# Kernel optimization log

Measured on AMD Instinct MI355X. Metric: run time of the kernel, lower is better.

Reference implementation:

```python
import jax, jax.numpy as jnp
import numpy as np

COMMITMENT_COST = 0.25


def setup_inputs() -> dict:
    key = jax.random.key(0)
    k1, k2 = jax.random.split(key)
    x = jax.random.normal(k1, (32, 256, 32, 32), dtype=jnp.float32)
    codebook = jax.random.normal(k2, (1024, 256), dtype=jnp.float32) * 0.02
    return {"x": x, "codebook": codebook}


def reference(x, codebook):
    # x: [B, C, H, W] -> z: [B, H, W, C] (NHWC), C = embedding_dim
    B, C, H, W = x.shape
    z = jnp.transpose(x, (0, 2, 3, 1))
    zf = z.reshape(-1, C)  # [N, C], N = B*H*W
    # squared euclidean distance: ||z||^2 - 2 z.e + ||e||^2  -> [N, K]
    d = (
        jnp.sum(zf * zf, axis=-1, keepdims=True)
        - 2.0 * (zf @ codebook.T)
        + jnp.sum(codebook * codebook, axis=-1)
    )
    encoding_indices = jnp.argmin(d, axis=1)  # [N]
    quantized = codebook[encoding_indices].reshape(z.shape)  # [B, H, W, C]

    # training losses (entropy_loss_ratio == 0 -> entropy branch skipped)
    sg = jax.lax.stop_gradient
    e_latent_loss = jnp.mean((sg(quantized) - z) ** 2) * COMMITMENT_COST
    q_latent_loss = jnp.mean((quantized - sg(z)) ** 2)
    quantizer_loss = e_latent_loss + q_latent_loss

    # straight-through estimator
    quantized_st = z + sg(quantized - z)
    out = jnp.transpose(quantized_st, (0, 3, 1, 2))  # back to NCHW
    return out, quantizer_loss, e_latent_loss, q_latent_loss, encoding_indices
```

## Files before the change

kernel.cpp:

```cpp
#include <hip/hip_runtime.h>
#include <cfloat>

#define C_DIM   256
#define HW      1024
#define N_ROWS  32768
#define K_CODES 1024
#define ROWS    64
#define NCHUNK  32
#define WCHUNK_BYTES 8192
#define LISTCAP 128
#define DELTA   0.008f
#define CMASK   0xFFFFFFE0u

#define OUT_ELEMS 8388608
#define LOSS_OFF  8388608
#define IDX_OFF   8388611

typedef _Float16 half8 __attribute__((ext_vector_type(8)));
typedef _Float16 f16x4 __attribute__((ext_vector_type(4)));
typedef float    f32x4 __attribute__((ext_vector_type(4)));

#define AS1 __attribute__((address_space(1)))
#define AS3 __attribute__((address_space(3)))

#define OFF_EBUF  0
#define OFF_EN    65536
#define OFF_S32   69632
#define OFF_M1W   69888
#define OFF_THR   70400
#define OFF_RES   70656
#define OFF_FIDX  71168
#define OFF_LCNT  71424
#define OFF_LMETA 71680
#define SMEM_BYTES 73728

#define QT_STRIDE 258

#define DPP_MIN(x, ctrl) fminf((x), __int_as_float(__builtin_amdgcn_update_dpp(0, __float_as_int(x), (ctrl), 0xf, 0xf, true)))

__global__ void prep_kernel(const float* __restrict__ cb, float* __restrict__ enorm,
                            char* __restrict__ cb16) {
    int k = blockIdx.x * 4 + (threadIdx.x >> 6);
    int lane = threadIdx.x & 63;
    int c0 = lane * 4;
    float4 v = *(const float4*)(cb + k * C_DIM + c0);
    double s = (double)v.x * v.x + (double)v.y * v.y + (double)v.z * v.z + (double)v.w * v.w;
    #pragma unroll
    for (int m = 1; m < 64; m <<= 1) s += __shfl_xor(s, m, 64);
    if (lane == 0) enorm[k] = (float)s;
    f16x4 h;
    h[0] = (_Float16)v.x; h[1] = (_Float16)v.y; h[2] = (_Float16)v.z; h[3] = (_Float16)v.w;
    int dst = ((k >> 4) << 13) + ((c0 >> 5) << 10) + (((c0 >> 3) & 3) << 8)
            + ((k & 15) << 4) + ((c0 & 7) << 1);
    *(f16x4*)(cb16 + dst) = h;
}

__global__ __launch_bounds__(256, 2) void vq_main(
    const float* __restrict__ x, const float* __restrict__ cb,
    const float* __restrict__ enorm_g, const char* __restrict__ cb16,
    float* __restrict__ out, float* __restrict__ idx_out, float* __restrict__ t2_out)
{
    extern __shared__ char smem[];
    float* qt      = (float*)(smem + OFF_EBUF);
    float* en_lds  = (float*)(smem + OFF_EN);
    float* S32     = (float*)(smem + OFF_S32);
    float* m1w     = (float*)(smem + OFF_M1W);
    float* thr     = (float*)(smem + OFF_THR);
    unsigned long long* res = (unsigned long long*)(smem + OFF_RES);
    int*   fidx    = (int*)(smem + OFF_FIDX);
    int*   lcnt    = (int*)(smem + OFF_LCNT);
    unsigned int* lmeta = (unsigned int*)(smem + OFF_LMETA);

    const int t    = threadIdx.x;
    const int lane = t & 63;
    const int wv   = t >> 6;
    const int wr   = wv >> 1;
    const int wc   = wv & 1;
    const int l15  = lane & 15;
    const int l4   = lane >> 4;
    const int row0 = blockIdx.x * ROWS;
    const int b    = row0 >> 10;
    const int hw0  = row0 & 1023;
    const float* xb = x + b * (C_DIM * HW) + hw0;

    char* ebw = smem + OFF_EBUF + wv * (2 * WCHUNK_BYTES);
    const char* cbw = cb16 + wc * WCHUNK_BYTES;

    #pragma unroll
    for (int c2 = 0; c2 < 2; c2++) {
        const char* src = cbw + (c2 << 14);
        char* dst = ebw + c2 * WCHUNK_BYTES;
        #pragma unroll
        for (int i = 0; i < 8; i++) {
            __builtin_amdgcn_global_load_lds((const AS1 unsigned int*)(src + i * 1024 + lane * 16),
                                             (AS3 unsigned int*)(dst + i * 1024), 16, 0, 0);
        }
    }

    *(float4*)&en_lds[t * 4] = *(const float4*)(enorm_g + t * 4);
    if (t < 4) lcnt[t] = 0;

    half8 af[2][8];
    double s64[2] = {0.0, 0.0};
    #pragma unroll
    for (int rt = 0; rt < 2; rt++) {
        const float* xr = xb + wr * 32 + rt * 16 + l15;
        #pragma unroll
        for (int kk = 0; kk < 8; kk++) {
            float v[8];
            #pragma unroll
            for (int j = 0; j < 8; j++) v[j] = xr[(kk * 32 + l4 * 8 + j) * HW];
            #pragma unroll
            for (int j = 0; j < 8; j++) s64[rt] = fma((double)v[j], (double)v[j], s64[rt]);
            half8 h;
            #pragma unroll
            for (int j = 0; j < 8; j++) h[j] = (_Float16)(-2.0f * v[j]);
            af[rt][kk] = h;
        }
    }
    #pragma unroll
    for (int rt = 0; rt < 2; rt++) {
        s64[rt] += __shfl_xor(s64[rt], 16, 64);
        s64[rt] += __shfl_xor(s64[rt], 32, 64);
    }
    if (l4 == 0 && wc == 0) {
        S32[wr * 32 + l15]      = (float)s64[0];
        S32[wr * 32 + 16 + l15] = (float)s64[1];
    }
    __syncthreads();

    const int bbase  = (l4 << 8) + (l15 << 4);
    const int enbase = wc * 16 + l15;

    float u1[2][4], u2[2][4];
    #pragma unroll
    for (int rt = 0; rt < 2; rt++)
        #pragma unroll
        for (int r2 = 0; r2 < 4; r2++) { u1[rt][r2] = FLT_MAX; u2[rt][r2] = FLT_MAX; }

    for (int ch = 0; ch < NCHUNK; ch++) {
        if (ch == NCHUNK - 1) { asm volatile("s_waitcnt vmcnt(0)" ::: "memory"); }
        else                  { asm volatile("s_waitcnt vmcnt(8)" ::: "memory"); }
        __builtin_amdgcn_sched_barrier(0);

        const char* ebc = ebw + (ch & 1) * WCHUNK_BYTES;
        half8 bf[8];
        #pragma unroll
        for (int kk = 0; kk < 8; kk++)
            bf[kk] = *(const half8*)(ebc + bbase + (kk << 10));
        asm volatile("s_waitcnt lgkmcnt(0)" ::: "memory");
        __builtin_amdgcn_sched_barrier(0);

        if (ch + 2 < NCHUNK) {
            const char* src = cbw + ((ch + 2) << 14);
            char* dst = ebw + (ch & 1) * WCHUNK_BYTES;
            #pragma unroll
            for (int i = 0; i < 8; i++) {
                __builtin_amdgcn_global_load_lds((const AS1 unsigned int*)(src + i * 1024 + lane * 16),
                                                 (AS3 unsigned int*)(dst + i * 1024), 16, 0, 0);
            }
        }

        const float en = en_lds[enbase + ch * 32];
        f32x4 acc0 = {en, en, en, en};
        f32x4 acc1 = {en, en, en, en};
        #pragma unroll
        for (int kk = 0; kk < 8; kk++) {
            acc0 = __builtin_amdgcn_mfma_f32_16x16x32_f16(af[0][kk], bf[kk], acc0, 0, 0, 0);
            acc1 = __builtin_amdgcn_mfma_f32_16x16x32_f16(af[1][kk], bf[kk], acc1, 0, 0, 0);
        }
        #pragma unroll
        for (int r2 = 0; r2 < 4; r2++) {
            float a0 = __uint_as_float((__float_as_uint(acc0[r2]) & CMASK) | (unsigned)ch);
            u2[0][r2] = __builtin_amdgcn_fmed3f(a0, u1[0][r2], u2[0][r2]);
            u1[0][r2] = fminf(u1[0][r2], a0);
            float a1 = __uint_as_float((__float_as_uint(acc1[r2]) & CMASK) | (unsigned)ch);
            u2[1][r2] = __builtin_amdgcn_fmed3f(a1, u1[1][r2], u2[1][r2]);
            u1[1][r2] = fminf(u1[1][r2], a1);
        }
    }

    #pragma unroll
    for (int rt = 0; rt < 2; rt++) {
        #pragma unroll
        for (int r2 = 0; r2 < 4; r2++) {
            float m = u1[rt][r2];
            m = DPP_MIN(m, 0xB1);
            m = DPP_MIN(m, 0x4E);
            m = DPP_MIN(m, 0x141);
            m = DPP_MIN(m, 0x140);
            if (l15 == 0) m1w[wc * 64 + wr * 32 + rt * 16 + l4 * 4 + r2] = m;
        }
    }
    __syncthreads();
    if (t < 64) {
        thr[t] = fminf(m1w[t], m1w[64 + t]) + DELTA;
        res[t] = ~0ull;
    }
    __syncthreads();

    #pragma unroll
    for (int rt = 0; rt < 2; rt++) {
        #pragma unroll
        for (int r2 = 0; r2 < 4; r2++) {
            int row_l = wr * 32 + rt * 16 + l4 * 4 + r2;
            float tr = thr[row_l];
            if (u1[rt][r2] < tr) {
                int ch1 = (int)(__float_as_uint(u1[rt][r2]) & 31u);
                int code = ch1 * 32 + wc * 16 + l15;
                int slot = atomicAdd(&lcnt[wv], 1);
                if (slot < LISTCAP)
                    lmeta[wv * LISTCAP + slot] = ((unsigned)row_l << 16) | (unsigned)code;
            }
            if (u2[rt][r2] < tr) {
                int ch2 = (int)(__float_as_uint(u2[rt][r2]) & 31u);
                int code = ch2 * 32 + wc * 16 + l15;
                int slot = atomicAdd(&lcnt[wv], 1);
                if (slot < LISTCAP)
                    lmeta[wv * LISTCAP + slot] = ((unsigned)row_l << 16) | (unsigned)code;
            }
        }
    }
    __syncthreads();

    {
        int n = lcnt[wv]; if (n > LISTCAP) n = LISTCAP;
        for (int base = 0; base < n; base += 4) {
            int it = base + l4;
            if (it < n) {
                unsigned meta = lmeta[wv * LISTCAP + it];
                int row  = (int)(meta >> 16);
                int code = (int)(meta & 1023u);
                const float* xr = xb + row;
                const float* er = cb + code * C_DIM;
                double acc = 0.0;
                #pragma unroll
                for (int s2 = 0; s2 < 16; s2++) {
                    int c = l15 + 16 * s2;
                    acc = fma((double)xr[(size_t)c * HW], (double)er[c], acc);
                }
                acc += __shfl_xor(acc, 1, 64);
                acc += __shfl_xor(acc, 2, 64);
                acc += __shfl_xor(acc, 4, 64);
                acc += __shfl_xor(acc, 8, 64);
                if (l15 == 0) {
                    float Mf = (float)acc;
                    float t2 = __fadd_rn(__fsub_rn(S32[row], __fmul_rn(2.0f, Mf)), en_lds[code]);
                    unsigned long long pk =
                        ((unsigned long long)__float_as_uint(t2) << 32) | (unsigned long long)(unsigned)code;
                    atomicMin(&res[row], pk);
                }
            }
        }
    }
    __syncthreads();

    if (t < 64) {
        unsigned long long v = res[t];
        int code = (int)(v & 1023u);
        fidx[t] = code;
        idx_out[row0 + t] = (float)code;
        t2_out[row0 + t] = __uint_as_float((unsigned)(v >> 32));
    }

    float* ob = out + b * (C_DIM * HW) + hw0;
    #pragma unroll
    for (int half = 0; half < 2; half++) {
        __syncthreads();
        for (int idx = t; idx < 32 * 64; idx += 256) {
            int r  = idx >> 6;
            int c4 = idx & 63;
            const float* er = cb + fidx[half * 32 + r] * C_DIM;
            *(float4*)&qt[r * QT_STRIDE + c4 * 4] = *(const float4*)(er + c4 * 4);
        }
        __syncthreads();
        int rr = t & 31;
        int cg = t >> 5;
        for (int cc = cg; cc < C_DIM; cc += 8) {
            ob[cc * HW + half * 32 + rr] = qt[rr * QT_STRIDE + cc];
        }
    }
}

__global__ void loss_kernel(const float* __restrict__ t2min, float* __restrict__ losses) {
    __shared__ double sh[256];
    int t = threadIdx.x;
    double a = 0.0;
    const int per = N_ROWS / 256;
    for (int i = t * per; i < t * per + per; i++) a += (double)t2min[i];
    sh[t] = a;
    __syncthreads();
    for (int s = 128; s > 0; s >>= 1) {
        if (t < s) sh[t] += sh[t + s];
        __syncthreads();
    }
    if (t == 0) {
        double M = sh[0] / (double)OUT_ELEMS;
        losses[0] = (float)(1.25 * M);
        losses[1] = (float)(0.25 * M);
        losses[2] = (float)(M);
    }
}

extern "C" void kernel_launch(void* const* d_in, const int* in_sizes, int n_in,
                              void* d_out, int out_size, void* d_ws, size_t ws_size,
                              hipStream_t stream) {
    const float* x  = (const float*)d_in[0];
    const float* cb = (const float*)d_in[1];
    float* out     = (float*)d_out;
    float* losses  = out + LOSS_OFF;
    float* idx_out = out + IDX_OFF;

    char*  cb16     = (char*)d_ws;
    float* t2ws     = (float*)((char*)d_ws + 524288);
    float* enorm_ws = (float*)((char*)d_ws + 524288 + 131072);

    hipFuncSetAttribute(reinterpret_cast<const void*>(vq_main),
                        hipFuncAttributeMaxDynamicSharedMemorySize, SMEM_BYTES);

    prep_kernel<<<K_CODES / 4, 256, 0, stream>>>(cb, enorm_ws, cb16);
    vq_main<<<N_ROWS / ROWS, 256, SMEM_BYTES, stream>>>(x, cb, enorm_ws, cb16, out, idx_out, t2ws);
    loss_kernel<<<1, 256, 0, stream>>>(t2ws, losses);
}
```

Baseline: 69.95 us.

## Stage x tile through LDS with vectorized loads before building MFMA fragments

The block's 64x256 input tile is now loaded with coalesced float4 global reads and transposed into a padded LDS buffer. The squared norms and the fp16 A fragments are then built from LDS, which replaces the old strided scalar loads that each wave issued separately. The codebook async-to-LDS copy now starts only after this staging finishes, because it reuses the same buffer region. This adds two barriers and 1 KB of shared memory, and it removes the overlap between the codebook prefetch and the x loads.

```diff
diff --git a/kernel.cpp b/kernel.cpp
--- a/kernel.cpp
+++ b/kernel.cpp
@@ -11,6 +11,7 @@
 #define LISTCAP 128
 #define DELTA   0.008f
 #define CMASK   0xFFFFFFE0u
+#define ZSTRIDE 260
 
 #define OUT_ELEMS 8388608
 #define LOSS_OFF  8388608
@@ -24,15 +25,15 @@
 #define AS3 __attribute__((address_space(3)))
 
 #define OFF_EBUF  0
-#define OFF_EN    65536
-#define OFF_S32   69632
-#define OFF_M1W   69888
-#define OFF_THR   70400
-#define OFF_RES   70656
-#define OFF_FIDX  71168
-#define OFF_LCNT  71424
-#define OFF_LMETA 71680
-#define SMEM_BYTES 73728
+#define OFF_EN    66560
+#define OFF_S32   70656
+#define OFF_M1W   70912
+#define OFF_THR   71424
+#define OFF_RES   71680
+#define OFF_FIDX  72192
+#define OFF_LCNT  72448
+#define OFF_LMETA 72704
+#define SMEM_BYTES 74752
 
 #define QT_STRIDE 258
 
@@ -61,6 +62,7 @@
     float* __restrict__ out, float* __restrict__ idx_out, float* __restrict__ t2_out)
 {
     extern __shared__ char smem[];
+    float* zt      = (float*)(smem + OFF_EBUF);
     float* qt      = (float*)(smem + OFF_EBUF);
     float* en_lds  = (float*)(smem + OFF_EN);
     float* S32     = (float*)(smem + OFF_S32);
@@ -86,6 +88,59 @@
     char* ebw = smem + OFF_EBUF + wv * (2 * WCHUNK_BYTES);
     const char* cbw = cb16 + wc * WCHUNK_BYTES;
 
+    {
+        int g   = t & 15;
+        int cb4 = t >> 4;
+        for (int cc = cb4 * 4; cc < C_DIM; cc += 64) {
+            float4 v0 = *(const float4*)(xb + (cc + 0) * HW + g * 4);
+            float4 v1 = *(const float4*)(xb + (cc + 1) * HW + g * 4);
+            float4 v2 = *(const float4*)(xb + (cc + 2) * HW + g * 4);
+            float4 v3 = *(const float4*)(xb + (cc + 3) * HW + g * 4);
+            *(float4*)&zt[(g * 4 + 0) * ZSTRIDE + cc] = make_float4(v0.x, v1.x, v2.x, v3.x);
+            *(float4*)&zt[(g * 4 + 1) * ZSTRIDE + cc] = make_float4(v0.y, v1.y, v2.y, v3.y);
+            *(float4*)&zt[(g * 4 + 2) * ZSTRIDE + cc] = make_float4(v0.z, v1.z, v2.z, v3.z);
+            *(float4*)&zt[(g * 4 + 3) * ZSTRIDE + cc] = make_float4(v0.w, v1.w, v2.w, v3.w);
+        }
+        *(float4*)&en_lds[t * 4] = *(const float4*)(enorm_g + t * 4);
+        if (t < 4) lcnt[t] = 0;
+    }
+    __syncthreads();
+
+    {
+        int r = t >> 2, seg = t & 3;
+        const float* zr = &zt[r * ZSTRIDE + seg * 64];
+        double s = 0.0;
+        for (int c = 0; c < 64; c += 4) {
+            float4 v = *(const float4*)(zr + c);
+            s = fma((double)v.x, (double)v.x, s);
+            s = fma((double)v.y, (double)v.y, s);
+            s = fma((double)v.z, (double)v.z, s);
+            s = fma((double)v.w, (double)v.w, s);
+        }
+        s += __shfl_xor(s, 1, 64);
+        s += __shfl_xor(s, 2, 64);
+        if (seg == 0) S32[r] = (float)s;
+    }
+
+    half8 af[2][8];
+    #pragma unroll
+    for (int rt = 0; rt < 2; rt++) {
+        int row = wr * 32 + rt * 16 + l15;
+        #pragma unroll
+        for (int kk = 0; kk < 8; kk++) {
+            int c0 = kk * 32 + l4 * 8;
+            float4 a  = *(const float4*)&zt[row * ZSTRIDE + c0];
+            float4 a2 = *(const float4*)&zt[row * ZSTRIDE + c0 + 4];
+            half8 h;
+            h[0] = (_Float16)(-2.0f * a.x);  h[1] = (_Float16)(-2.0f * a.y);
+            h[2] = (_Float16)(-2.0f * a.z);  h[3] = (_Float16)(-2.0f * a.w);
+            h[4] = (_Float16)(-2.0f * a2.x); h[5] = (_Float16)(-2.0f * a2.y);
+            h[6] = (_Float16)(-2.0f * a2.z); h[7] = (_Float16)(-2.0f * a2.w);
+            af[rt][kk] = h;
+        }
+    }
+    __syncthreads();
+
     #pragma unroll
     for (int c2 = 0; c2 < 2; c2++) {
         const char* src = cbw + (c2 << 14);
@@ -96,38 +151,6 @@
                                              (AS3 unsigned int*)(dst + i * 1024), 16, 0, 0);
         }
     }
-
-    *(float4*)&en_lds[t * 4] = *(const float4*)(enorm_g + t * 4);
-    if (t < 4) lcnt[t] = 0;
-
-    half8 af[2][8];
-    double s64[2] = {0.0, 0.0};
-    #pragma unroll
-    for (int rt = 0; rt < 2; rt++) {
-        const float* xr = xb + wr * 32 + rt * 16 + l15;
-        #pragma unroll
-        for (int kk = 0; kk < 8; kk++) {
-            float v[8];
-            #pragma unroll
-            for (int j = 0; j < 8; j++) v[j] = xr[(kk * 32 + l4 * 8 + j) * HW];
-            #pragma unroll
-            for (int j = 0; j < 8; j++) s64[rt] = fma((double)v[j], (double)v[j], s64[rt]);
-            half8 h;
-            #pragma unroll
-            for (int j = 0; j < 8; j++) h[j] = (_Float16)(-2.0f * v[j]);
-            af[rt][kk] = h;
-        }
-    }
-    #pragma unroll
-    for (int rt = 0; rt < 2; rt++) {
-        s64[rt] += __shfl_xor(s64[rt], 16, 64);
-        s64[rt] += __shfl_xor(s64[rt], 32, 64);
-    }
-    if (l4 == 0 && wc == 0) {
-        S32[wr * 32 + l15]      = (float)s64[0];
-        S32[wr * 32 + 16 + l15] = (float)s64[1];
-    }
-    __syncthreads();
 
     const int bbase  = (l4 << 8) + (l15 << 4);
     const int enbase = wc * 16 + l15;
```

After: 69.00 us. About the same (-1.4%).
